# Performance work log

Measured on AMD Instinct MI355X. Metric: run time of the kernel, lower is better.

Reference implementation:

```python
import jax, jax.numpy as jnp
import numpy as np

D = 1024; H = 1024; B = 4; S = 2048
BASE_COUPLING = 0.1
NUM_ADAPTIVE_CYCLES = 3
EPS = 1e-5


def layer_norm(x, g, b):
    m = jnp.mean(x, axis=-1, keepdims=True)
    v = jnp.var(x, axis=-1, keepdims=True)
    return (x - m) * jax.lax.rsqrt(v + EPS) * g + b


def linear(x, W, b):
    return x @ W.T + b


def gelu(x):
    return jax.nn.gelu(x, approximate=False)  # torch nn.GELU default (erf)


def gru_layer(x, W_ih, W_hh, b_ih, b_hh):
    # x: (B,S,Din). torch nn.GRU cell math, h0 = 0.
    b, s, _ = x.shape
    h_dim = W_hh.shape[1]
    xi = jnp.einsum('bsd,gd->bsg', x, W_ih) + b_ih  # (B,S,3H) precomputed input GEMM

    def step(h, xt):
        hh = h @ W_hh.T + b_hh
        xr, xz, xn = jnp.split(xt, 3, axis=-1)
        hr, hz, hn = jnp.split(hh, 3, axis=-1)
        r = jax.nn.sigmoid(xr + hr)
        z = jax.nn.sigmoid(xz + hz)
        n = jnp.tanh(xn + r * hn)
        h_new = (1.0 - z) * n + z * h
        return h_new, h_new

    h0 = jnp.zeros((b, h_dim), x.dtype)
    _, ys = jax.lax.scan(step, h0, jnp.swapaxes(xi, 0, 1))
    return jnp.swapaxes(ys, 0, 1)  # (B,S,H)


def mobius_twist(x):
    # x: (...,D), D % 4 == 0. quarters [a,b,c,d] -> [c,-d,-a,b]
    q = x.shape[-1] // 4
    a, bq, c, d = jnp.split(x, 4, axis=-1)
    return jnp.concatenate([c, -d, -a, bq], axis=-1)


def coupling_mlp(x, cw1, cb1, cw2, cb2, cw3, cb3, cw4, cb4):
    h = gelu(linear(x, cw1, cb1))
    h = gelu(linear(h, cw2, cb2))
    h = gelu(linear(h, cw3, cb3))
    return jax.nn.sigmoid(linear(h, cw4, cb4))  # (...,1)


def global_mlp(x, gw1, gb1, gw2, gb2, gw3, gb3):
    h = gelu(linear(x, gw1, gb1))
    h = gelu(linear(h, gw2, gb2))
    return jax.nn.sigmoid(linear(h, gw3, gb3))  # (B,1,1)


def adaptive_mobius(x, cw1, cb1, cw2, cb2, cw3, cb3, cw4, cb4,
                    gw1, gb1, gw2, gb2, gw3, gb3, adaptive_range):
    gc = x.mean(axis=1, keepdims=True)                       # (B,1,D)
    g = global_mlp(gc, gw1, gb1, gw2, gb2, gw3, gb3)         # (B,1,1)
    out = x
    for _ in range(NUM_ADAPTIVE_CYCLES):
        tf = coupling_mlp(out, cw1, cb1, cw2, cb2, cw3, cb3, cw4, cb4)  # (B,S,1)
        combined = 0.7 * g + 0.3 * tf
        coup = BASE_COUPLING + adaptive_range * (combined - 0.5) * 2.0
        out = out + coup * mobius_twist(out)  # vectorized over all timesteps
    return out


def setup_inputs() -> dict:
    key = jax.random.key(0)
    ks = jax.random.split(key, 24)

    def w(k, shape, s=0.02):
        return jax.random.normal(k, shape, dtype=jnp.float32) * s

    return {
        'x': jax.random.normal(ks[0], (B, S, D), dtype=jnp.float32),
        'g1w': jnp.ones((D,), jnp.float32), 'g1b': jnp.zeros((D,), jnp.float32),
        'g2w': jnp.ones((D,), jnp.float32), 'g2b': jnp.zeros((D,), jnp.float32),
        'W_ih0': w(ks[1], (3 * H, D)), 'W_hh0': w(ks[2], (3 * H, H)),
        'b_ih0': jnp.zeros((3 * H,), jnp.float32), 'b_hh0': jnp.zeros((3 * H,), jnp.float32),
        'W_ih1': w(ks[3], (3 * H, H)), 'W_hh1': w(ks[4], (3 * H, H)),
        'b_ih1': jnp.zeros((3 * H,), jnp.float32), 'b_hh1': jnp.zeros((3 * H,), jnp.float32),
        'cw1': w(ks[5], (D, D)), 'cb1': jnp.zeros((D,), jnp.float32),
        'cw2': w(ks[6], (D // 2, D)), 'cb2': jnp.zeros((D // 2,), jnp.float32),
        'cw3': w(ks[7], (D // 4, D // 2)), 'cb3': jnp.zeros((D // 4,), jnp.float32),
        'cw4': w(ks[8], (1, D // 4)), 'cb4': jnp.zeros((1,), jnp.float32),
        'gw1': w(ks[9], (D // 2, D)), 'gb1': jnp.zeros((D // 2,), jnp.float32),
        'gw2': w(ks[10], (D // 4, D // 2)), 'gb2': jnp.zeros((D // 4,), jnp.float32),
        'gw3': w(ks[11], (1, D // 4)), 'gb3': jnp.zeros((1,), jnp.float32),
        'adaptive_range': jnp.ones((1,), jnp.float32) * 0.2,
        'fw1': w(ks[12], (4 * D, D)), 'fb1': jnp.zeros((4 * D,), jnp.float32),
        'fw2': w(ks[13], (D, 4 * D)), 'fb2': jnp.zeros((D,), jnp.float32),
    }


def reference(x, g1w, g1b, g2w, g2b,
              W_ih0, W_hh0, b_ih0, b_hh0, W_ih1, W_hh1, b_ih1, b_hh1,
              cw1, cb1, cw2, cb2, cw3, cb3, cw4, cb4,
              gw1, gb1, gw2, gb2, gw3, gb3, adaptive_range,
              fw1, fb1, fw2, fb2):
    # Block 1: norm -> recurrent (2-layer GRU stand-in for TwistorTitansRecurrent) -> residual
    res = x
    h = layer_norm(x, g1w, g1b)
    h = gru_layer(h, W_ih0, W_hh0, b_ih0, b_hh0)
    h = gru_layer(h, W_ih1, W_hh1, b_ih1, b_hh1)
    x = res + h  # output_proj is Identity (hidden_dim == dim)

    # Block 2: norm -> adaptive mobius -> residual
    res = x
    h = layer_norm(x, g2w, g2b)
    h = adaptive_mobius(h, cw1, cb1, cw2, cb2, cw3, cb3, cw4, cb4,
                        gw1, gb1, gw2, gb2, gw3, gb3, adaptive_range)
    x = res + h

    # Block 3: FFN residual (eval mode: dropout off, no self_modify scaling)
    x = x + linear(gelu(linear(x, fw1, fb1)), fw2, fb2)
    return x
```

## Files before the change

### kernel.cpp

```cpp
#include <hip/hip_runtime.h>
#include <math.h>

#define D_DIM 1024
#define S_LEN 2048
#define B_SZ  4
#define GRU_BLOCKS 256

union F4 { float4 v; float f[4]; };
typedef float v2f __attribute__((ext_vector_type(2)));
union U64 { v2f v; unsigned long long u; float f[2]; };

__device__ __forceinline__ float gelu_f(float x) {
  return 0.5f * x * (1.0f + erff(x * 0.70710678118654752440f));
}
__device__ __forceinline__ float sigmoid_f(float x) {
  return __fdividef(1.0f, 1.0f + __expf(-x));
}
__device__ __forceinline__ float tanh_f(float x) {
  const float xc = fminf(fmaxf(x, -15.0f), 15.0f);
  const float a = __expf(2.0f * xc);
  return __fdividef(a - 1.0f, a + 1.0f);
}

__global__ __launch_bounds__(256) void ln_kernel(
    const float* __restrict__ x, const float* __restrict__ gamma,
    const float* __restrict__ beta, float* __restrict__ out) {
  const int row = blockIdx.x;
  const int tid = threadIdx.x;
  const int wave = tid >> 6, lane = tid & 63;
  const float4 v = ((const float4*)(x + (size_t)row * D_DIM))[tid];
  float s  = v.x + v.y + v.z + v.w;
  float ss = v.x * v.x + v.y * v.y + v.z * v.z + v.w * v.w;
#pragma unroll
  for (int m = 1; m < 64; m <<= 1) {
    s  += __shfl_xor(s,  m, 64);
    ss += __shfl_xor(ss, m, 64);
  }
  __shared__ float r0[4], r1[4];
  if (lane == 0) { r0[wave] = s; r1[wave] = ss; }
  __syncthreads();
  s  = r0[0] + r0[1] + r0[2] + r0[3];
  ss = r1[0] + r1[1] + r1[2] + r1[3];
  const float mean = s * (1.0f / D_DIM);
  const float var  = ss * (1.0f / D_DIM) - mean * mean;
  const float inv  = rsqrtf(var + 1e-5f);
  const float4 g4 = ((const float4*)gamma)[tid];
  const float4 b4 = ((const float4*)beta)[tid];
  float4 o;
  o.x = (v.x - mean) * inv * g4.x + b4.x;
  o.y = (v.y - mean) * inv * g4.y + b4.y;
  o.z = (v.z - mean) * inv * g4.z + b4.z;
  o.w = (v.w - mean) * inv * g4.w + b4.w;
  ((float4*)(out + (size_t)row * D_DIM))[tid] = o;
}

#define BM 128
#define BN 128
#define BKK 8
#define TM 8
#define TN 8
__global__ __launch_bounds__(256) void gemm_kernel(
    const float* __restrict__ A, int lda,
    const float* __restrict__ W, int ldw,
    const float* __restrict__ bias,
    const float* __restrict__ res,
    float* __restrict__ C,
    int M, int N, int K, int act) {
  __shared__ float As[BKK][BM];
  __shared__ float Bs[BKK][BN];
  const int tid = threadIdx.x;
  const int bm = blockIdx.y * BM;
  const int bn = blockIdx.x * BN;
  const int tx = tid & 15;
  const int ty = tid >> 4;
  const int lrow = tid >> 1;
  const int lk = (tid & 1) * 4;
  const float* Ag = A + (size_t)(bm + lrow) * lda + lk;
  const float* Wg = W + (size_t)(bn + lrow) * ldw + lk;

  v2f acc2[TM][TN / 2];
#pragma unroll
  for (int i = 0; i < TM; ++i)
#pragma unroll
    for (int j = 0; j < TN / 2; ++j) acc2[i][j] = (v2f){0.0f, 0.0f};

  for (int k0 = 0; k0 < K; k0 += BKK) {
    const float4 av = *(const float4*)(Ag + k0);
    const float4 wv = *(const float4*)(Wg + k0);
    __syncthreads();
    As[lk + 0][lrow] = av.x; As[lk + 1][lrow] = av.y;
    As[lk + 2][lrow] = av.z; As[lk + 3][lrow] = av.w;
    Bs[lk + 0][lrow] = wv.x; Bs[lk + 1][lrow] = wv.y;
    Bs[lk + 2][lrow] = wv.z; Bs[lk + 3][lrow] = wv.w;
    __syncthreads();
#pragma unroll
    for (int k = 0; k < BKK; ++k) {
      F4 a0, a1, b0, b1;
      a0.v = *(const float4*)(&As[k][ty * TM]);
      a1.v = *(const float4*)(&As[k][ty * TM + 4]);
      b0.v = *(const float4*)(&Bs[k][tx * TN]);
      b1.v = *(const float4*)(&Bs[k][tx * TN + 4]);
      float a[TM] = {a0.f[0], a0.f[1], a0.f[2], a0.f[3],
                     a1.f[0], a1.f[1], a1.f[2], a1.f[3]};
      v2f b2[TN / 2] = {(v2f){b0.f[0], b0.f[1]}, (v2f){b0.f[2], b0.f[3]},
                        (v2f){b1.f[0], b1.f[1]}, (v2f){b1.f[2], b1.f[3]}};
#pragma unroll
      for (int i = 0; i < TM; ++i) {
        const v2f asp = (v2f){a[i], a[i]};
#pragma unroll
        for (int j = 0; j < TN / 2; ++j)
          acc2[i][j] = __builtin_elementwise_fma(asp, b2[j], acc2[i][j]);
      }
    }
  }

  float bs_[TN];
#pragma unroll
  for (int j = 0; j < TN; ++j) bs_[j] = bias ? bias[bn + tx * TN + j] : 0.0f;
#pragma unroll
  for (int i = 0; i < TM; ++i) {
    const size_t coff = (size_t)(bm + ty * TM + i) * N + bn + tx * TN;
    float vals[TN];
#pragma unroll
    for (int j = 0; j < TN / 2; ++j) {
#pragma unroll
      for (int e = 0; e < 2; ++e) {
        float v = acc2[i][j][e] + bs_[j * 2 + e];
        if (act == 1) v = gelu_f(v);
        vals[j * 2 + e] = v;
      }
    }
    if (res) {
#pragma unroll
      for (int j = 0; j < TN; ++j) vals[j] += res[coff + j];
    }
    *(float4*)(C + coff)     = make_float4(vals[0], vals[1], vals[2], vals[3]);
    *(float4*)(C + coff + 4) = make_float4(vals[4], vals[5], vals[6], vals[7]);
  }
}

__global__ __launch_bounds__(512, 2) void gru2_kernel(
    const float* __restrict__ xi,
    const float* __restrict__ Whh0,
    const float* __restrict__ bhh0,
    const float* __restrict__ Wih1,
    const float* __restrict__ bih1,
    const float* __restrict__ Whh1,
    const float* __restrict__ bhh1,
    const float* __restrict__ resid,
    float* __restrict__ y,
    float* __restrict__ h1buf,
    float* __restrict__ h2buf,
    unsigned* __restrict__ slots)
{
  const int tid = threadIdx.x;
  const int wave = tid >> 6, lane = tid & 63;
  const int jj = wave & 3;
  const int j = (blockIdx.x << 2) + jj;
  const int p = (wave >> 2) << 1;

  __shared__ float h1_lds[4096];
  __shared__ float h2_lds[4096];
  __shared__ float wb_lds[12288];

  v2f wa0[3][4][2], wa1[3][4][2];
#pragma unroll
  for (int g = 0; g < 3; ++g) {
#pragma unroll
    for (int c = 0; c < 4; ++c) {
      F4 q0; q0.v = *(const float4*)(Whh0 + (size_t)(g * 1024 + j) * 1024 + (c << 8) + (lane << 2));
      wa0[g][c][0] = (v2f){q0.f[0], q0.f[1]};
      wa0[g][c][1] = (v2f){q0.f[2], q0.f[3]};
      F4 q1; q1.v = *(const float4*)(Whh1 + (size_t)(g * 1024 + j) * 1024 + (c << 8) + (lane << 2));
      wa1[g][c][0] = (v2f){q1.f[0], q1.f[1]};
      wa1[g][c][1] = (v2f){q1.f[2], q1.f[3]};
    }
  }
  if (wave < 4) {
#pragma unroll
    for (int g = 0; g < 3; ++g)
#pragma unroll
      for (int c = 0; c < 4; ++c) {
        const float4 q = *(const float4*)(Wih1 + (size_t)(g * 1024 + j) * 1024 + (c << 8) + (lane << 2));
        ((float4*)wb_lds)[(((jj * 3 + g) << 2) + c) * 64 + lane] = q;
      }
  }
  const float b1r = bhh0[j], b1z = bhh0[1024 + j], b1hn = bhh0[2048 + j];
  const float b2r  = bih1[j] + bhh1[j];
  const float b2z  = bih1[1024 + j] + bhh1[1024 + j];
  const float b2in = bih1[2048 + j];
  const float b2hn = bhh1[2048 + j];

  float hold1[2] = {0.0f, 0.0f};
  float hold2[2] = {0.0f, 0.0f};

  float xr[2], xz[2], xn[2];
#pragma unroll
  for (int bb = 0; bb < 2; ++bb) {
    const float* xp = xi + ((size_t)((p + bb) * S_LEN)) * 3072 + j;
    xr[bb] = xp[0]; xz[bb] = xp[1024]; xn[bb] = xp[2048];
  }

  for (int s = 0; s <= S_LEN; ++s) {
    float* hr1 = h1buf + ((s & 1) << 12);
    float* hw1 = h1buf + (((s + 1) & 1) << 12);
    float* hr2 = h2buf + (((s + 1) & 1) << 12);
    float* hw2 = h2buf + ((s & 1) << 12);

    {
      const int tt = tid & 255;
      const float* bsrc = (tid < 256) ? hr1 : hr2;
      const float* p0 = bsrc + (tt << 2);
      float4 r0, r1, r2, r3;
      asm volatile("global_load_dwordx4 %0, %1, off sc0 sc1" : "=v"(r0) : "v"(p0));
      asm volatile("global_load_dwordx4 %0, %1, off sc0 sc1" : "=v"(r1) : "v"(p0 + 1024));
      asm volatile("global_load_dwordx4 %0, %1, off sc0 sc1" : "=v"(r2) : "v"(p0 + 2048));
      asm volatile("global_load_dwordx4 %0, %1, off sc0 sc1" : "=v"(r3) : "v"(p0 + 3072));
      asm volatile("s_waitcnt vmcnt(0)" ::: "memory");
      __builtin_amdgcn_sched_barrier(0);
      float* dl = (tid < 256) ? h1_lds : h2_lds;
      ((float4*)dl)[tt]       = r0;
      ((float4*)dl)[tt + 256] = r1;
      ((float4*)dl)[tt + 512] = r2;
      ((float4*)dl)[tt + 768] = r3;
    }
    __syncthreads();

    float nxr[2], nxz[2], nxn[2];
    {
      const int tn = (s + 1 < S_LEN) ? (s + 1) : (S_LEN - 1);
#pragma unroll
      for (int bb = 0; bb < 2; ++bb) {
        const float* xp = xi + ((size_t)((p + bb) * S_LEN + tn)) * 3072 + j;
        nxr[bb] = xp[0]; nxz[bb] = xp[1024]; nxn[bb] = xp[2048];
      }
    }

    v2f aA[3][2], aX[3][2], aH[3][2];
#pragma unroll
    for (int g = 0; g < 3; ++g)
#pragma unroll
      for (int bb = 0; bb < 2; ++bb) {
        aA[g][bb] = (v2f){0.f, 0.f};
        aX[g][bb] = (v2f){0.f, 0.f};
        aH[g][bb] = (v2f){0.f, 0.f};
      }
#pragma unroll
    for (int c = 0; c < 4; ++c) {
      v2f wb_[3][2];
#pragma unroll
      for (int g = 0; g < 3; ++g) {
        F4 w; w.v = ((const float4*)wb_lds)[(((jj * 3 + g) << 2) + c) * 64 + lane];
        wb_[g][0] = (v2f){w.f[0], w.f[1]};
        wb_[g][1] = (v2f){w.f[2], w.f[3]};
      }
#pragma unroll
      for (int bb = 0; bb < 2; ++bb) {
        F4 q1; q1.v = *((const float4*)(h1_lds + ((p + bb) << 10) + (c << 8)) + lane);
        F4 q2; q2.v = *((const float4*)(h2_lds + ((p + bb) << 10) + (c << 8)) + lane);
        const v2f h1lo = (v2f){q1.f[0], q1.f[1]}, h1hi = (v2f){q1.f[2], q1.f[3]};
        const v2f h2lo = (v2f){q2.f[0], q2.f[1]}, h2hi = (v2f){q2.f[2], q2.f[3]};
#pragma unroll
        for (int g = 0; g < 3; ++g) {
          aA[g][bb] = __builtin_elementwise_fma(wa0[g][c][0], h1lo, aA[g][bb]);
          aA[g][bb] = __builtin_elementwise_fma(wa0[g][c][1], h1hi, aA[g][bb]);
          aX[g][bb] = __builtin_elementwise_fma(wb_[g][0],   h1lo, aX[g][bb]);
          aX[g][bb] = __builtin_elementwise_fma(wb_[g][1],   h1hi, aX[g][bb]);
          aH[g][bb] = __builtin_elementwise_fma(wa1[g][c][0], h2lo, aH[g][bb]);
          aH[g][bb] = __builtin_elementwise_fma(wa1[g][c][1], h2hi, aH[g][bb]);
        }
      }
    }
    v2f A0, A1, A2, V0, V1, V2, V3;
    A0 = (v2f){aA[0][0][0] + aA[0][0][1], aA[0][1][0] + aA[0][1][1]};
    A1 = (v2f){aA[1][0][0] + aA[1][0][1], aA[1][1][0] + aA[1][1][1]};
    A2 = (v2f){aA[2][0][0] + aA[2][0][1], aA[2][1][0] + aA[2][1][1]};
    V0 = (v2f){aX[0][0][0] + aX[0][0][1] + aH[0][0][0] + aH[0][0][1],
               aX[0][1][0] + aX[0][1][1] + aH[0][1][0] + aH[0][1][1]};
    V1 = (v2f){aX[1][0][0] + aX[1][0][1] + aH[1][0][0] + aH[1][0][1],
               aX[1][1][0] + aX[1][1][1] + aH[1][1][0] + aH[1][1][1]};
    V2 = (v2f){aX[2][0][0] + aX[2][0][1], aX[2][1][0] + aX[2][1][1]};
    V3 = (v2f){aH[2][0][0] + aH[2][0][1], aH[2][1][0] + aH[2][1][1]};
#pragma unroll
    for (int m = 1; m < 64; m <<= 1) {
      U64 t;
      t.v = A0; t.u = __shfl_xor(t.u, m, 64); A0 += t.v;
      t.v = A1; t.u = __shfl_xor(t.u, m, 64); A1 += t.v;
      t.v = A2; t.u = __shfl_xor(t.u, m, 64); A2 += t.v;
      t.v = V0; t.u = __shfl_xor(t.u, m, 64); V0 += t.v;
      t.v = V1; t.u = __shfl_xor(t.u, m, 64); V1 += t.v;
      t.v = V2; t.u = __shfl_xor(t.u, m, 64); V2 += t.v;
      t.v = V3; t.u = __shfl_xor(t.u, m, 64); V3 += t.v;
    }

    if (s < S_LEN) {
#pragma unroll
      for (int bb = 0; bb < 2; ++bb) {
        const float r = sigmoid_f(xr[bb] + A0[bb] + b1r);
        const float z = sigmoid_f(xz[bb] + A1[bb] + b1z);
        const float n = tanh_f(xn[bb] + r * (A2[bb] + b1hn));
        hold1[bb] = (1.0f - z) * n + z * hold1[bb];
      }
      if (lane < 2) {
        const float sv = (lane == 0) ? hold1[0] : hold1[1];
        __hip_atomic_store(hw1 + ((p + lane) << 10) + j, sv,
                           __ATOMIC_RELAXED, __HIP_MEMORY_SCOPE_AGENT);
      }
    }
    if (s >= 1) {
#pragma unroll
      for (int bb = 0; bb < 2; ++bb) {
        const float r = sigmoid_f(V0[bb] + b2r);
        const float z = sigmoid_f(V1[bb] + b2z);
        const float n = tanh_f(V2[bb] + b2in + r * (V3[bb] + b2hn));
        hold2[bb] = (1.0f - z) * n + z * hold2[bb];
      }
      if (lane < 2) {
        const float sv = (lane == 0) ? hold2[0] : hold2[1];
        __hip_atomic_store(hw2 + ((p + lane) << 10) + j, sv,
                           __ATOMIC_RELAXED, __HIP_MEMORY_SCOPE_AGENT);
      }
    }

    __syncthreads();
    if (tid == 0)
      __hip_atomic_store(slots + (blockIdx.x << 4), (unsigned)(s + 1),
                         __ATOMIC_RELAXED, __HIP_MEMORY_SCOPE_AGENT);
    if (s >= 1 && lane < 2) {
      const float sv = (lane == 0) ? hold2[0] : hold2[1];
      const size_t oidx = ((size_t)((p + lane) * S_LEN + (s - 1))) * 1024 + j;
      y[oidx] = sv + resid[oidx];
    }
    {
      const unsigned target = (unsigned)(s + 1);
      for (;;) {
        const unsigned q0 = __hip_atomic_load(slots + ((lane      ) << 4),
                             __ATOMIC_RELAXED, __HIP_MEMORY_SCOPE_AGENT);
        const unsigned q1 = __hip_atomic_load(slots + ((lane +  64) << 4),
                             __ATOMIC_RELAXED, __HIP_MEMORY_SCOPE_AGENT);
        const unsigned q2 = __hip_atomic_load(slots + ((lane + 128) << 4),
                             __ATOMIC_RELAXED, __HIP_MEMORY_SCOPE_AGENT);
        const unsigned q3 = __hip_atomic_load(slots + ((lane + 192) << 4),
                             __ATOMIC_RELAXED, __HIP_MEMORY_SCOPE_AGENT);
        unsigned m01 = q0 < q1 ? q0 : q1;
        unsigned m23 = q2 < q3 ? q2 : q3;
        unsigned mm = m01 < m23 ? m01 : m23;
        if (__all(mm >= target)) break;
        __builtin_amdgcn_s_sleep(1);
      }
    }

#pragma unroll
    for (int bb = 0; bb < 2; ++bb) {
      xr[bb] = nxr[bb]; xz[bb] = nxz[bb]; xn[bb] = nxn[bb];
    }
  }
}

__global__ __launch_bounds__(256) void colmean_kernel(
    const float* __restrict__ in, float* __restrict__ gc) {
  const int b = blockIdx.x >> 3, tc = blockIdx.x & 7;
  const int d = threadIdx.x;
  float s0 = 0.f, s1 = 0.f, s2 = 0.f, s3 = 0.f;
  const float* base = in + ((size_t)b * S_LEN + tc * 256) * D_DIM;
  for (int t = 0; t < 256; ++t) {
    const float* r = base + (size_t)t * D_DIM;
    s0 += r[d]; s1 += r[d + 256]; s2 += r[d + 512]; s3 += r[d + 768];
  }
  const float sc = 1.0f / (float)S_LEN;
  atomicAdd(&gc[b * D_DIM + d], s0 * sc);
  atomicAdd(&gc[b * D_DIM + d + 256], s1 * sc);
  atomicAdd(&gc[b * D_DIM + d + 512], s2 * sc);
  atomicAdd(&gc[b * D_DIM + d + 768], s3 * sc);
}

__global__ __launch_bounds__(256) void gmlp_kernel(
    const float* __restrict__ gc,
    const float* __restrict__ gw1, const float* __restrict__ gb1,
    const float* __restrict__ gw2, const float* __restrict__ gb2,
    const float* __restrict__ gw3, const float* __restrict__ gb3,
    float* __restrict__ gout) {
  const int b = blockIdx.x, tid = threadIdx.x;
  __shared__ float xin[1024];
  __shared__ float h1[512];
  __shared__ float h2[256];
#pragma unroll
  for (int i = 0; i < 4; ++i) xin[tid + i * 256] = gc[b * 1024 + tid + i * 256];
  __syncthreads();
  for (int o = tid; o < 512; o += 256) {
    const float* wr = gw1 + (size_t)o * 1024;
    float acc = gb1[o];
    for (int k = 0; k < 1024; k += 4) {
      const float4 wv = *(const float4*)(wr + k);
      acc += wv.x * xin[k] + wv.y * xin[k + 1] + wv.z * xin[k + 2] + wv.w * xin[k + 3];
    }
    h1[o] = gelu_f(acc);
  }
  __syncthreads();
  {
    const float* wr = gw2 + (size_t)tid * 512;
    float acc = gb2[tid];
    for (int k = 0; k < 512; k += 4) {
      const float4 wv = *(const float4*)(wr + k);
      acc += wv.x * h1[k] + wv.y * h1[k + 1] + wv.z * h1[k + 2] + wv.w * h1[k + 3];
    }
    h2[tid] = gelu_f(acc);
  }
  __syncthreads();
  float p = h2[tid] * gw3[tid];
#pragma unroll
  for (int m = 1; m < 64; m <<= 1) p += __shfl_xor(p, m, 64);
  __shared__ float rr[4];
  if ((tid & 63) == 0) rr[tid >> 6] = p;
  __syncthreads();
  if (tid == 0) gout[b] = sigmoid_f(rr[0] + rr[1] + rr[2] + rr[3] + gb3[0]);
}

__global__ __launch_bounds__(256) void gemv_sig_kernel(
    const float* __restrict__ A, const float* __restrict__ w,
    const float* __restrict__ bias, float* __restrict__ out) {
  const int row = blockIdx.x * 4 + (threadIdx.x >> 6);
  const int lane = threadIdx.x & 63;
  F4 a, wv;
  a.v  = ((const float4*)(A + (size_t)row * 256))[lane];
  wv.v = ((const float4*)w)[lane];
  float p = a.f[0] * wv.f[0] + a.f[1] * wv.f[1] + a.f[2] * wv.f[2] + a.f[3] * wv.f[3];
#pragma unroll
  for (int m = 1; m < 64; m <<= 1) p += __shfl_xor(p, m, 64);
  if (lane == 0) out[row] = sigmoid_f(p + bias[0]);
}

__global__ __launch_bounds__(256) void mobius_kernel(
    float* __restrict__ out, const float* __restrict__ tf,
    const float* __restrict__ g, const float* __restrict__ ar,
    const float* __restrict__ res) {
  const int idx = blockIdx.x * 256 + threadIdx.x;
  const int row = idx >> 9;
  const int d = idx & 511;
  const int b = row >> 11;
  const float combined = 0.7f * g[b] + 0.3f * tf[row];
  const float coup = 0.1f + ar[0] * (combined - 0.5f) * 2.0f;
  float* base = out + (size_t)row * 1024;
  const float f = base[d], s2 = base[d + 512];
  const float sgn = (d < 256) ? 1.0f : -1.0f;
  float nf = f + sgn * coup * s2;
  float ns = s2 - sgn * coup * f;
  if (res) {
    const float* rb = res + (size_t)row * 1024;
    nf += rb[d];
    ns += rb[d + 512];
  }
  base[d] = nf;
  base[d + 512] = ns;
}

extern "C" void kernel_launch(void* const* d_in, const int* in_sizes, int n_in,
                              void* d_out, int out_size, void* d_ws, size_t ws_size,
                              hipStream_t stream) {
  (void)in_sizes; (void)n_in; (void)out_size; (void)ws_size;
  const float* x    = (const float*)d_in[0];
  const float* g1w  = (const float*)d_in[1];
  const float* g1b  = (const float*)d_in[2];
  const float* g2w  = (const float*)d_in[3];
  const float* g2b  = (const float*)d_in[4];
  const float* Wih0 = (const float*)d_in[5];
  const float* Whh0 = (const float*)d_in[6];
  const float* bih0 = (const float*)d_in[7];
  const float* bhh0 = (const float*)d_in[8];
  const float* Wih1 = (const float*)d_in[9];
  const float* Whh1 = (const float*)d_in[10];
  const float* bih1 = (const float*)d_in[11];
  const float* bhh1 = (const float*)d_in[12];
  const float* cw1 = (const float*)d_in[13]; const float* cb1 = (const float*)d_in[14];
  const float* cw2 = (const float*)d_in[15]; const float* cb2 = (const float*)d_in[16];
  const float* cw3 = (const float*)d_in[17]; const float* cb3 = (const float*)d_in[18];
  const float* cw4 = (const float*)d_in[19]; const float* cb4 = (const float*)d_in[20];
  const float* gw1 = (const float*)d_in[21]; const float* gb1 = (const float*)d_in[22];
  const float* gw2 = (const float*)d_in[23]; const float* gb2 = (const float*)d_in[24];
  const float* gw3 = (const float*)d_in[25]; const float* gb3 = (const float*)d_in[26];
  const float* ar  = (const float*)d_in[27];
  const float* fw1 = (const float*)d_in[28]; const float* fb1 = (const float*)d_in[29];
  const float* fw2 = (const float*)d_in[30]; const float* fb2 = (const float*)d_in[31];
  float* outp = (float*)d_out;

  float* A  = (float*)d_ws;
  float* Bb = A + 25165824;
  float* small = Bb + 8388608;
  float* gc   = small;
  float* gbuf = small + 4096;
  float* tf   = small + 4104;
  float* hb0  = small + 12296;
  float* hb1  = small + 20488;
  unsigned* slots0 = (unsigned*)(small + 28680);
  hipMemsetAsync(small, 0, (size_t)(36872 + 64) * sizeof(float), stream);

  ln_kernel<<<8192, 256, 0, stream>>>(x, g1w, g1b, Bb);
  gemm_kernel<<<dim3(24, 64), 256, 0, stream>>>(Bb, 1024, Wih0, 1024, bih0, nullptr,
                                                A, 8192, 3072, 1024, 0);
  gru2_kernel<<<GRU_BLOCKS, 512, 0, stream>>>(A, Whh0, bhh0, Wih1, bih1,
                                              Whh1, bhh1, x, outp,
                                              hb0, hb1, slots0);

  ln_kernel<<<8192, 256, 0, stream>>>(outp, g2w, g2b, Bb);
  colmean_kernel<<<32, 256, 0, stream>>>(Bb, gc);
  gmlp_kernel<<<4, 256, 0, stream>>>(gc, gw1, gb1, gw2, gb2, gw3, gb3, gbuf);
  float* c1o = A;
  float* c2o = A + 12582912;
  float* c3o = A + 20971520;
  for (int cyc = 0; cyc < 3; ++cyc) {
    gemm_kernel<<<dim3(8, 64), 256, 0, stream>>>(Bb, 1024, cw1, 1024, cb1, nullptr,
                                                 c1o, 8192, 1024, 1024, 1);
    gemm_kernel<<<dim3(4, 64), 256, 0, stream>>>(c1o, 1024, cw2, 1024, cb2, nullptr,
                                                 c2o, 8192, 512, 1024, 1);
    gemm_kernel<<<dim3(2, 64), 256, 0, stream>>>(c2o, 512, cw3, 512, cb3, nullptr,
                                                 c3o, 8192, 256, 512, 1);
    gemv_sig_kernel<<<2048, 256, 0, stream>>>(c3o, cw4, cb4, tf);
    mobius_kernel<<<16384, 256, 0, stream>>>(Bb, tf, gbuf, ar,
                                             (cyc == 2) ? outp : nullptr);
  }

  for (int c = 0; c < 2; ++c) {
    gemm_kernel<<<dim3(16, 64), 256, 0, stream>>>(Bb, 1024,
        fw1 + (size_t)c * 2048 * 1024, 1024, fb1 + c * 2048, nullptr,
        A, 8192, 2048, 1024, 1);
    gemm_kernel<<<dim3(8, 64), 256, 0, stream>>>(A, 2048,
        fw2 + c * 2048, 4096, (c == 0) ? fb2 : nullptr,
        (c == 0) ? Bb : outp,
        outp, 8192, 1024, 2048, 0);
  }
}
```

Baseline: 15.02 ms.

## Split GRU grid into independent batch-pair groups with per-group barriers

The fused two-layer GRU kernel's 256 blocks are repartitioned into two independent groups of 128 blocks, one per batch pair. Each block now covers 8 hidden units for 2 batches instead of 4 units for 4 batches. Each step then reloads only half the hidden state into LDS, and the grid barrier spans 128 blocks instead of 256. Only wave 0 polls the global slots and then releases the other waves through an LDS flag, which cuts global atomic traffic. In exchange, LDS use rises to about 112KB per block because every wave now stages its own Wih1 rows, which limits residency to one block per CU.

Measured after the change: 13.45 ms. 10.4% less time.

```diff
diff --git a/kernel.cpp b/kernel.cpp
--- a/kernel.cpp
+++ b/kernel.cpp
@@ -155,13 +155,18 @@
 {
   const int tid = threadIdx.x;
   const int wave = tid >> 6, lane = tid & 63;
-  const int jj = wave & 3;
-  const int j = (blockIdx.x << 2) + jj;
-  const int p = (wave >> 2) << 1;
-
-  __shared__ float h1_lds[4096];
-  __shared__ float h2_lds[4096];
-  __shared__ float wb_lds[12288];
+  const int gid  = blockIdx.x >> 7;
+  const int gbid = blockIdx.x & 127;
+  const int j = (gbid << 3) + wave;
+  const int p = gid << 1;
+  unsigned* myslots = slots + (gid << 11);
+
+  __shared__ float h1_lds[2048];
+  __shared__ float h2_lds[2048];
+  __shared__ float wb_lds[24576];
+  __shared__ unsigned flag;
+
+  if (tid == 0) flag = 0u;
 
   v2f wa0[3][4][2], wa1[3][4][2];
 #pragma unroll
@@ -176,15 +181,13 @@
       wa1[g][c][1] = (v2f){q1.f[2], q1.f[3]};
     }
   }
-  if (wave < 4) {
-#pragma unroll
-    for (int g = 0; g < 3; ++g)
-#pragma unroll
-      for (int c = 0; c < 4; ++c) {
-        const float4 q = *(const float4*)(Wih1 + (size_t)(g * 1024 + j) * 1024 + (c << 8) + (lane << 2));
-        ((float4*)wb_lds)[(((jj * 3 + g) << 2) + c) * 64 + lane] = q;
-      }
-  }
+#pragma unroll
+  for (int g = 0; g < 3; ++g)
+#pragma unroll
+    for (int c = 0; c < 4; ++c) {
+      const float4 q = *(const float4*)(Wih1 + (size_t)(g * 1024 + j) * 1024 + (c << 8) + (lane << 2));
+      ((float4*)wb_lds)[(((wave * 3 + g) << 2) + c) * 64 + lane] = q;
+    }
   const float b1r = bhh0[j], b1z = bhh0[1024 + j], b1hn = bhh0[2048 + j];
   const float b2r  = bih1[j] + bhh1[j];
   const float b2z  = bih1[1024 + j] + bhh1[1024 + j];
@@ -209,20 +212,15 @@
 
     {
       const int tt = tid & 255;
-      const float* bsrc = (tid < 256) ? hr1 : hr2;
-      const float* p0 = bsrc + (tt << 2);
-      float4 r0, r1, r2, r3;
-      asm volatile("global_load_dwordx4 %0, %1, off sc0 sc1" : "=v"(r0) : "v"(p0));
-      asm volatile("global_load_dwordx4 %0, %1, off sc0 sc1" : "=v"(r1) : "v"(p0 + 1024));
-      asm volatile("global_load_dwordx4 %0, %1, off sc0 sc1" : "=v"(r2) : "v"(p0 + 2048));
-      asm volatile("global_load_dwordx4 %0, %1, off sc0 sc1" : "=v"(r3) : "v"(p0 + 3072));
+      const float* bsrc = ((tid < 256) ? hr1 : hr2) + (p << 10) + (tt << 2);
+      float4 r0, r1;
+      asm volatile("global_load_dwordx4 %0, %1, off sc0 sc1" : "=v"(r0) : "v"(bsrc));
+      asm volatile("global_load_dwordx4 %0, %1, off sc0 sc1" : "=v"(r1) : "v"(bsrc + 1024));
       asm volatile("s_waitcnt vmcnt(0)" ::: "memory");
       __builtin_amdgcn_sched_barrier(0);
       float* dl = (tid < 256) ? h1_lds : h2_lds;
       ((float4*)dl)[tt]       = r0;
       ((float4*)dl)[tt + 256] = r1;
-      ((float4*)dl)[tt + 512] = r2;
-      ((float4*)dl)[tt + 768] = r3;
     }
     __syncthreads();
 
@@ -250,14 +248,14 @@
       v2f wb_[3][2];
 #pragma unroll
       for (int g = 0; g < 3; ++g) {
-        F4 w; w.v = ((const float4*)wb_lds)[(((jj * 3 + g) << 2) + c) * 64 + lane];
+        F4 w; w.v = ((const float4*)wb_lds)[(((wave * 3 + g) << 2) + c) * 64 + lane];
         wb_[g][0] = (v2f){w.f[0], w.f[1]};
         wb_[g][1] = (v2f){w.f[2], w.f[3]};
       }
 #pragma unroll
       for (int bb = 0; bb < 2; ++bb) {
-        F4 q1; q1.v = *((const float4*)(h1_lds + ((p + bb) << 10) + (c << 8)) + lane);
-        F4 q2; q2.v = *((const float4*)(h2_lds + ((p + bb) << 10) + (c << 8)) + lane);
+        F4 q1; q1.v = *((const float4*)(h1_lds + (bb << 10) + (c << 8)) + lane);
+        F4 q2; q2.v = *((const float4*)(h2_lds + (bb << 10) + (c << 8)) + lane);
         const v2f h1lo = (v2f){q1.f[0], q1.f[1]}, h1hi = (v2f){q1.f[2], q1.f[3]};
         const v2f h2lo = (v2f){q2.f[0], q2.f[1]}, h2hi = (v2f){q2.f[2], q2.f[3]};
 #pragma unroll
@@ -324,7 +322,7 @@
 
     __syncthreads();
     if (tid == 0)
-      __hip_atomic_store(slots + (blockIdx.x << 4), (unsigned)(s + 1),
+      __hip_atomic_store(myslots + (gbid << 4), (unsigned)(s + 1),
                          __ATOMIC_RELAXED, __HIP_MEMORY_SCOPE_AGENT);
     if (s >= 1 && lane < 2) {
       const float sv = (lane == 0) ? hold2[0] : hold2[1];
@@ -333,20 +331,21 @@
     }
     {
       const unsigned target = (unsigned)(s + 1);
-      for (;;) {
-        const unsigned q0 = __hip_atomic_load(slots + ((lane      ) << 4),
-                             __ATOMIC_RELAXED, __HIP_MEMORY_SCOPE_AGENT);
-        const unsigned q1 = __hip_atomic_load(slots + ((lane +  64) << 4),
-                             __ATOMIC_RELAXED, __HIP_MEMORY_SCOPE_AGENT);
-        const unsigned q2 = __hip_atomic_load(slots + ((lane + 128) << 4),
-                             __ATOMIC_RELAXED, __HIP_MEMORY_SCOPE_AGENT);
-        const unsigned q3 = __hip_atomic_load(slots + ((lane + 192) << 4),
-                             __ATOMIC_RELAXED, __HIP_MEMORY_SCOPE_AGENT);
-        unsigned m01 = q0 < q1 ? q0 : q1;
-        unsigned m23 = q2 < q3 ? q2 : q3;
-        unsigned mm = m01 < m23 ? m01 : m23;
-        if (__all(mm >= target)) break;
-        __builtin_amdgcn_s_sleep(1);
+      if (wave == 0) {
+        for (;;) {
+          const unsigned q0 = __hip_atomic_load(myslots + ((lane     ) << 4),
+                               __ATOMIC_RELAXED, __HIP_MEMORY_SCOPE_AGENT);
+          const unsigned q1 = __hip_atomic_load(myslots + ((lane + 64) << 4),
+                               __ATOMIC_RELAXED, __HIP_MEMORY_SCOPE_AGENT);
+          const unsigned mm = q0 < q1 ? q0 : q1;
+          if (__all(mm >= target)) break;
+          __builtin_amdgcn_s_sleep(1);
+        }
+        __hip_atomic_store(&flag, target, __ATOMIC_RELAXED,
+                           __HIP_MEMORY_SCOPE_WORKGROUP);
+      } else {
+        while (__hip_atomic_load(&flag, __ATOMIC_RELAXED,
+                                 __HIP_MEMORY_SCOPE_WORKGROUP) < target) {}
       }
     }
 
```
